# Kernel optimization log

Hardware: AMD Instinct MI355X
Metric: run time of the kernel (lower is better)

Reference implementation:

```python
import jax, jax.numpy as jnp
import numpy as np

B, HQ, HK, S, D, HID, BS = 2, 32, 8, 8192, 128, 128, 16
NB = S // BS  # 512 pooled blocks


def rotate_half(x):
    h = x.shape[-1] // 2
    return jnp.concatenate([-x[..., h:], x[..., :h]], axis=-1)


def pool_cat(x):
    # avg + max pooling over block_size along the sequence dim, concat on feature dim
    b, h, s, d = x.shape
    xb = x.reshape(b, h, s // BS, BS, d)
    return jnp.concatenate([xb.mean(axis=3), xb.max(axis=3)], axis=-1)  # [b,h,NB,2d]


def setup_inputs() -> dict:
    key = jax.random.key(0)
    k0, k1, k2, k3 = jax.random.split(key, 4)
    q = jax.random.normal(k0, (B, HQ, S, D), jnp.float32)
    k = jax.random.normal(k1, (B, HK, S, D), jnp.float32)
    wq = jax.random.normal(k2, (HQ, 2 * D, HID), jnp.float32) / np.float32(np.sqrt(2 * D))
    wk = jax.random.normal(k3, (HK, 2 * D, HID), jnp.float32) / np.float32(np.sqrt(2 * D))
    # causal block mask
    mask = jnp.broadcast_to(jnp.tril(jnp.ones((NB, NB), bool))[None, None], (B, 1, NB, NB))
    # RoPE tables over pooled positions
    pos = jnp.arange(NB, dtype=jnp.float32)
    inv_freq = 1.0 / (10000.0 ** (jnp.arange(0, HID, 2, dtype=jnp.float32) / HID))
    freqs = pos[:, None] * inv_freq[None, :]              # [NB, HID/2]
    emb = jnp.concatenate([freqs, freqs], axis=-1)        # [NB, HID]
    cos = jnp.broadcast_to(jnp.cos(emb)[None], (B, NB, HID))
    sin = jnp.broadcast_to(jnp.sin(emb)[None], (B, NB, HID))
    return {"q": q, "k": k, "attention_mask": mask, "cos": cos, "sin": sin, "wq": wq, "wk": wk}


def reference(q, k, attention_mask, cos, sin, wq, wk):
    # pooled multi-head linear projections
    qh = jnp.einsum('bhnc,hcd->bhnd', pool_cat(q), wq)   # [B,HQ,NB,HID]
    kh = jnp.einsum('bhnc,hcd->bhnd', pool_cat(k), wk)   # [B,HK,NB,HID]
    # RoPE (unsqueeze_dim=1)
    c, s = cos[:, None], sin[:, None]
    qh = qh * c + rotate_half(qh) * s
    kh = kh * c + rotate_half(kh) * s
    # GQA: repeat kv heads
    kh = jnp.repeat(kh, HQ // HK, axis=1)                # [B,HQ,NB,HID]
    attn = jnp.einsum('bhqd,bhkd->bhqk', qh, kh) / jnp.sqrt(jnp.float32(HID))
    attn = jnp.where(attention_mask, attn, jnp.float32(-1e9))
    return jax.nn.softmax(attn, axis=-1)
```

## Files before the change

### kernel.cpp

```cpp
#include <hip/hip_runtime.h>

namespace {
constexpr int BB  = 2;
constexpr int HQ  = 32;
constexpr int HK  = 8;
constexpr int S   = 8192;
constexpr int D   = 128;
constexpr int HID = 128;
constexpr int BS  = 16;
constexpr int NB  = 512;
constexpr int C2D = 256;
}

__global__ __launch_bounds__(256) void pool_gemm_rope_kernel(
    const float* __restrict__ qx, const float* __restrict__ kx,
    const float* __restrict__ wqp, const float* __restrict__ wkp,
    const float* __restrict__ cosp, const float* __restrict__ sinp,
    float* __restrict__ qh, float* __restrict__ kh)
{
  constexpr int PST = 260;
  constexpr int RST = 132;
  __shared__ float smem[32 * PST];

  const int t  = threadIdx.x;
  const int n0 = blockIdx.x * 32;
  const int hy = blockIdx.y;
  const int b  = blockIdx.z;

  const float* x; const float* w; float* o; int H; int h;
  if (hy < HQ) { x = qx; w = wqp; o = qh; H = HQ; h = hy; }
  else         { x = kx; w = wkp; o = kh; H = HK; h = hy - HQ; }

  const float* xb = x + (((size_t)b * H + h) * S + (size_t)n0 * BS) * D;
  for (int it = t; it < 32 * 32; it += 256) {
    const int m = it >> 5, d4 = it & 31;
    const float4* p = (const float4*)(xb + (size_t)m * BS * D) + d4;
    float4 v = p[0];
    float sx = v.x, sy = v.y, sz = v.z, sw = v.w;
    float mx = v.x, my = v.y, mz = v.z, mw = v.w;
#pragma unroll
    for (int i = 1; i < BS; ++i) {
      v = p[i * (D / 4)];
      sx += v.x; sy += v.y; sz += v.z; sw += v.w;
      mx = fmaxf(mx, v.x); my = fmaxf(my, v.y);
      mz = fmaxf(mz, v.z); mw = fmaxf(mw, v.w);
    }
    const float inv16 = 1.0f / 16.0f;
    *(float4*)&smem[m * PST + 4 * d4] =
        make_float4(sx * inv16, sy * inv16, sz * inv16, sw * inv16);
    *(float4*)&smem[m * PST + 128 + 4 * d4] = make_float4(mx, my, mz, mw);
  }
  __syncthreads();

  const int dt = t & 31, mt = t >> 5;
  const int d0 = dt * 4, m0 = mt * 4;
  const float* wb = w + (size_t)h * C2D * HID;
  float4 acc[4];
#pragma unroll
  for (int i = 0; i < 4; ++i) acc[i] = make_float4(0.f, 0.f, 0.f, 0.f);

  for (int c = 0; c < C2D; c += 4) {
    const float4 w0 = *(const float4*)(wb + (size_t)(c + 0) * HID + d0);
    const float4 w1 = *(const float4*)(wb + (size_t)(c + 1) * HID + d0);
    const float4 w2 = *(const float4*)(wb + (size_t)(c + 2) * HID + d0);
    const float4 w3 = *(const float4*)(wb + (size_t)(c + 3) * HID + d0);
#pragma unroll
    for (int i = 0; i < 4; ++i) {
      const float4 pv = *(const float4*)&smem[(m0 + i) * PST + c];
      acc[i].x += pv.x * w0.x + pv.y * w1.x + pv.z * w2.x + pv.w * w3.x;
      acc[i].y += pv.x * w0.y + pv.y * w1.y + pv.z * w2.y + pv.w * w3.y;
      acc[i].z += pv.x * w0.z + pv.y * w1.z + pv.z * w2.z + pv.w * w3.z;
      acc[i].w += pv.x * w0.w + pv.y * w1.w + pv.z * w2.w + pv.w * w3.w;
    }
  }
  __syncthreads();

#pragma unroll
  for (int i = 0; i < 4; ++i)
    *(float4*)&smem[(m0 + i) * RST + d0] = acc[i];
  __syncthreads();

  const float sgn = (d0 < 64) ? -1.0f : 1.0f;
#pragma unroll
  for (int i = 0; i < 4; ++i) {
    const int n = n0 + m0 + i;
    const float4 cv = *(const float4*)(cosp + ((size_t)b * NB + n) * HID + d0);
    const float4 sv = *(const float4*)(sinp + ((size_t)b * NB + n) * HID + d0);
    const float4 pr = *(const float4*)&smem[(m0 + i) * RST + (d0 ^ 64)];
    float4 ov;
    ov.x = acc[i].x * cv.x + sgn * pr.x * sv.x;
    ov.y = acc[i].y * cv.y + sgn * pr.y * sv.y;
    ov.z = acc[i].z * cv.z + sgn * pr.z * sv.z;
    ov.w = acc[i].w * cv.w + sgn * pr.w * sv.w;
    *(float4*)(o + (((size_t)b * H + h) * NB + n) * HID + d0) = ov;
  }
}

#define SWZ(r, d4) ((r) * 128 + ((((d4) ^ ((r) & 7))) << 2))

__global__ __launch_bounds__(256) void attn_exp_kernel(
    const float* __restrict__ qh, const float* __restrict__ kh,
    float* __restrict__ out, float* __restrict__ rinv)
{
  __shared__ float qs[64 * 128];
  __shared__ float ks[64 * 128];

  const int t = threadIdx.x;
  const int x = blockIdx.x;
  const int h = blockIdx.y;
  const int b = blockIdx.z;
  const int qg = t >> 4, kg = t & 15;
  const float scale = 0.08838834764831843f;

  const float* qbase = qh + (((size_t)b * HQ + h) * NB) * HID;
  const float* kbase = kh + (((size_t)b * HK + (h >> 2)) * NB) * HID;
  float* obase = out + (((size_t)b * HQ + h) * NB) * (size_t)NB;

  const int sq = qg & 7;
  const int sk = kg & 7;

  for (int sel = 0; sel < 2; ++sel) {
    const int qt = sel ? (7 - x) : x;
    __syncthreads();
    for (int it = t; it < 64 * 32; it += 256) {
      const int r = it >> 5, d4 = it & 31;
      *(float4*)&qs[SWZ(r, d4)] =
          *(const float4*)(qbase + ((size_t)(qt * 64 + r)) * HID + 4 * d4);
    }
    float rs[4] = {0.f, 0.f, 0.f, 0.f};

    for (int kt = 0; kt <= qt; ++kt) {
      __syncthreads();
      for (int it = t; it < 64 * 32; it += 256) {
        const int r = it >> 5, d4 = it & 31;
        *(float4*)&ks[SWZ(r, d4)] =
            *(const float4*)(kbase + ((size_t)(kt * 64 + r)) * HID + 4 * d4);
      }
      __syncthreads();

      float acc[4][4];
#pragma unroll
      for (int i = 0; i < 4; ++i)
#pragma unroll
        for (int j = 0; j < 4; ++j) acc[i][j] = 0.f;

      for (int d4 = 0; d4 < 32; ++d4) {
        const int xq = ((d4 ^ sq) << 2);
        const int xk = ((d4 ^ sk) << 2);
        float4 qv[4], kv[4];
#pragma unroll
        for (int i = 0; i < 4; ++i) qv[i] = *(const float4*)&qs[(qg + 16 * i) * 128 + xq];
#pragma unroll
        for (int j = 0; j < 4; ++j) kv[j] = *(const float4*)&ks[(kg + 16 * j) * 128 + xk];
#pragma unroll
        for (int i = 0; i < 4; ++i)
#pragma unroll
          for (int j = 0; j < 4; ++j)
            acc[i][j] += qv[i].x * kv[j].x + qv[i].y * kv[j].y +
                         qv[i].z * kv[j].z + qv[i].w * kv[j].w;
      }

      const bool diag = (kt == qt);
#pragma unroll
      for (int i = 0; i < 4; ++i) {
        const int qn = qt * 64 + qg + 16 * i;
#pragma unroll
        for (int j = 0; j < 4; ++j) {
          const int kn = kt * 64 + kg + 16 * j;
          float p = 0.0f;
          if (!diag || kn <= qn) p = __expf(acc[i][j] * scale);
          rs[i] += p;
          obase[(size_t)qn * NB + kn] = p;
        }
      }
    }

#pragma unroll
    for (int i = 0; i < 4; ++i) {
      float v = rs[i];
      v += __shfl_xor(v, 1, 64);
      v += __shfl_xor(v, 2, 64);
      v += __shfl_xor(v, 4, 64);
      v += __shfl_xor(v, 8, 64);
      if (kg == 0)
        rinv[((size_t)b * HQ + h) * NB + qt * 64 + qg + 16 * i] = 1.0f / v;
    }
  }
}

__global__ __launch_bounds__(128) void norm_kernel(
    float* __restrict__ out, const float* __restrict__ rinv)
{
  const int qn = blockIdx.x, h = blockIdx.y, b = blockIdx.z;
  const size_t row = ((size_t)b * HQ + h) * NB + qn;
  const float inv = rinv[row];
  const int klim4 = ((qn >> 6) + 1) * 16;
  float4* orow = (float4*)(out + row * NB);
  const int j = threadIdx.x;
  float4 v;
  if (j < klim4) {
    v = orow[j];
    v.x *= inv; v.y *= inv; v.z *= inv; v.w *= inv;
  } else {
    v = make_float4(0.f, 0.f, 0.f, 0.f);
  }
  orow[j] = v;
}

extern "C" void kernel_launch(void* const* d_in, const int* in_sizes, int n_in,
                              void* d_out, int out_size, void* d_ws, size_t ws_size,
                              hipStream_t stream)
{
  const float* q    = (const float*)d_in[0];
  const float* k    = (const float*)d_in[1];
  const float* cosp = (const float*)d_in[3];
  const float* sinp = (const float*)d_in[4];
  const float* wq   = (const float*)d_in[5];
  const float* wk   = (const float*)d_in[6];
  float* out = (float*)d_out;

  float* qh   = (float*)d_ws;
  float* kh   = qh + (size_t)BB * HQ * NB * HID;
  float* rinv = kh + (size_t)BB * HK * NB * HID;

  hipLaunchKernelGGL(pool_gemm_rope_kernel, dim3(NB / 32, HQ + HK, BB), dim3(256),
                     0, stream, q, k, wq, wk, cosp, sinp, qh, kh);
  hipLaunchKernelGGL(attn_exp_kernel, dim3(4, HQ, BB), dim3(256),
                     0, stream, qh, kh, out, rinv);
  hipLaunchKernelGGL(norm_kernel, dim3(NB, HQ, BB), dim3(128),
                     0, stream, out, rinv);
}
```

Baseline: 534.8 us.

## Use split-bf16 MFMA for attention scores and fuse normalization into attention kernel

The projection kernel now writes Q/K as hi+lo bf16 pairs, with the softmax scale folded into Q. The attention kernel computes scores with 16x16x32 bf16 MFMA using three products (hi*hi, hi*lo, lo*hi) to approximate fp32 accuracy. Row sums are reduced through LDS inside the block, and probabilities are kept in registers so they can be normalized before the single store. This removes the separate norm kernel and its re-read of the output. Work is split into 16-row strips paired for causal balance, and the masked region is zero-filled. The cost is a small precision loss from the split-bf16 approximation and scattered 4-byte output stores.

New measurement: 487.2 us. 8.9% less time.

```diff
diff --git a/kernel.cpp b/kernel.cpp
--- a/kernel.cpp
+++ b/kernel.cpp
@@ -10,13 +10,27 @@
 constexpr int BS  = 16;
 constexpr int NB  = 512;
 constexpr int C2D = 256;
+constexpr int RW  = 256;
+}
+
+typedef __attribute__((ext_vector_type(8))) short short8;
+typedef __attribute__((ext_vector_type(4))) float f32x4;
+
+__device__ inline unsigned short f2bf(float f) {
+  unsigned u = __builtin_bit_cast(unsigned, f);
+  unsigned r = u + 0x7fff + ((u >> 16) & 1);
+  return (unsigned short)(r >> 16);
+}
+__device__ inline float bf2f(unsigned short s) {
+  unsigned u = ((unsigned)s) << 16;
+  return __builtin_bit_cast(float, u);
 }
 
 __global__ __launch_bounds__(256) void pool_gemm_rope_kernel(
     const float* __restrict__ qx, const float* __restrict__ kx,
     const float* __restrict__ wqp, const float* __restrict__ wkp,
     const float* __restrict__ cosp, const float* __restrict__ sinp,
-    float* __restrict__ qh, float* __restrict__ kh)
+    unsigned short* __restrict__ qhb, unsigned short* __restrict__ khb)
 {
   constexpr int PST = 260;
   constexpr int RST = 132;
@@ -27,9 +41,9 @@
   const int hy = blockIdx.y;
   const int b  = blockIdx.z;
 
-  const float* x; const float* w; float* o; int H; int h;
-  if (hy < HQ) { x = qx; w = wqp; o = qh; H = HQ; h = hy; }
-  else         { x = kx; w = wkp; o = kh; H = HK; h = hy - HQ; }
+  const float* x; const float* w; unsigned short* o; int H; int h; bool isq;
+  if (hy < HQ) { x = qx; w = wqp; o = qhb; H = HQ; h = hy; isq = true; }
+  else         { x = kx; w = wkp; o = khb; H = HK; h = hy - HQ; isq = false; }
 
   const float* xb = x + (((size_t)b * H + h) * S + (size_t)n0 * BS) * D;
   for (int it = t; it < 32 * 32; it += 256) {
@@ -81,130 +95,135 @@
   __syncthreads();
 
   const float sgn = (d0 < 64) ? -1.0f : 1.0f;
+  const float qscale = isq ? 0.08838834764831843f : 1.0f;
 #pragma unroll
   for (int i = 0; i < 4; ++i) {
     const int n = n0 + m0 + i;
     const float4 cv = *(const float4*)(cosp + ((size_t)b * NB + n) * HID + d0);
     const float4 sv = *(const float4*)(sinp + ((size_t)b * NB + n) * HID + d0);
     const float4 pr = *(const float4*)&smem[(m0 + i) * RST + (d0 ^ 64)];
-    float4 ov;
-    ov.x = acc[i].x * cv.x + sgn * pr.x * sv.x;
-    ov.y = acc[i].y * cv.y + sgn * pr.y * sv.y;
-    ov.z = acc[i].z * cv.z + sgn * pr.z * sv.z;
-    ov.w = acc[i].w * cv.w + sgn * pr.w * sv.w;
-    *(float4*)(o + (((size_t)b * H + h) * NB + n) * HID + d0) = ov;
-  }
-}
-
-#define SWZ(r, d4) ((r) * 128 + ((((d4) ^ ((r) & 7))) << 2))
-
-__global__ __launch_bounds__(256) void attn_exp_kernel(
-    const float* __restrict__ qh, const float* __restrict__ kh,
-    float* __restrict__ out, float* __restrict__ rinv)
+    float ov[4];
+    ov[0] = (acc[i].x * cv.x + sgn * pr.x * sv.x) * qscale;
+    ov[1] = (acc[i].y * cv.y + sgn * pr.y * sv.y) * qscale;
+    ov[2] = (acc[i].z * cv.z + sgn * pr.z * sv.z) * qscale;
+    ov[3] = (acc[i].w * cv.w + sgn * pr.w * sv.w) * qscale;
+    ushort4 hi, lo;
+    hi.x = f2bf(ov[0]); lo.x = f2bf(ov[0] - bf2f(hi.x));
+    hi.y = f2bf(ov[1]); lo.y = f2bf(ov[1] - bf2f(hi.y));
+    hi.z = f2bf(ov[2]); lo.z = f2bf(ov[2] - bf2f(hi.z));
+    hi.w = f2bf(ov[3]); lo.w = f2bf(ov[3] - bf2f(hi.w));
+    unsigned short* orow = o + (((size_t)b * H + h) * NB + n) * RW + d0;
+    *(ushort4*)orow = hi;
+    *(ushort4*)(orow + 128) = lo;
+  }
+}
+
+__global__ __launch_bounds__(256) void attn_kernel(
+    const unsigned short* __restrict__ qhb,
+    const unsigned short* __restrict__ khb,
+    float* __restrict__ out)
 {
-  __shared__ float qs[64 * 128];
-  __shared__ float ks[64 * 128];
+  __shared__ float rs_lds[16];
 
   const int t = threadIdx.x;
+  const int w = t >> 6;
+  const int lane = t & 63;
+  const int col = lane & 15;
+  const int quad = lane >> 4;
   const int x = blockIdx.x;
   const int h = blockIdx.y;
   const int b = blockIdx.z;
-  const int qg = t >> 4, kg = t & 15;
-  const float scale = 0.08838834764831843f;
-
-  const float* qbase = qh + (((size_t)b * HQ + h) * NB) * HID;
-  const float* kbase = kh + (((size_t)b * HK + (h >> 2)) * NB) * HID;
+
+  const unsigned short* qbase = qhb + (((size_t)b * HQ + h) * NB) * RW;
+  const unsigned short* kbase = khb + (((size_t)b * HK + (h >> 2)) * NB) * RW;
   float* obase = out + (((size_t)b * HQ + h) * NB) * (size_t)NB;
 
-  const int sq = qg & 7;
-  const int sk = kg & 7;
-
-  for (int sel = 0; sel < 2; ++sel) {
-    const int qt = sel ? (7 - x) : x;
+  for (int ph = 0; ph < 2; ++ph) {
+    const int strip = ph ? (31 - x) : x;
+
     __syncthreads();
-    for (int it = t; it < 64 * 32; it += 256) {
-      const int r = it >> 5, d4 = it & 31;
-      *(float4*)&qs[SWZ(r, d4)] =
-          *(const float4*)(qbase + ((size_t)(qt * 64 + r)) * HID + 4 * d4);
-    }
+    if (t < 16) rs_lds[t] = 0.f;
+    __syncthreads();
+
+    const unsigned short* qrow = qbase + (size_t)(strip * 16 + col) * RW + quad * 8;
+    short8 qf[8];
+#pragma unroll
+    for (int f = 0; f < 4; ++f) {
+      qf[f]     = *(const short8*)(qrow + f * 32);
+      qf[4 + f] = *(const short8*)(qrow + f * 32 + 128);
+    }
+
+    const unsigned short* krow = kbase + (size_t)col * RW + quad * 8;
+    const int n = (w <= strip) ? ((strip - w) >> 2) + 1 : 0;
+
+    f32x4 pbuf[8];
     float rs[4] = {0.f, 0.f, 0.f, 0.f};
 
-    for (int kt = 0; kt <= qt; ++kt) {
-      __syncthreads();
-      for (int it = t; it < 64 * 32; it += 256) {
-        const int r = it >> 5, d4 = it & 31;
-        *(float4*)&ks[SWZ(r, d4)] =
-            *(const float4*)(kbase + ((size_t)(kt * 64 + r)) * HID + 4 * d4);
+#pragma unroll
+    for (int ti = 0; ti < 8; ++ti) {
+      if (ti < n) {
+        const int k16 = w + 4 * ti;
+        const unsigned short* kr = krow + (size_t)k16 * 16 * RW;
+        short8 kf[8];
+#pragma unroll
+        for (int f = 0; f < 4; ++f) {
+          kf[f]     = *(const short8*)(kr + f * 32);
+          kf[4 + f] = *(const short8*)(kr + f * 32 + 128);
+        }
+        f32x4 acc = {0.f, 0.f, 0.f, 0.f};
+#pragma unroll
+        for (int f = 0; f < 4; ++f) {
+          acc = __builtin_amdgcn_mfma_f32_16x16x32_bf16(qf[f],     kf[f],     acc, 0, 0, 0);
+          acc = __builtin_amdgcn_mfma_f32_16x16x32_bf16(qf[f],     kf[4 + f], acc, 0, 0, 0);
+          acc = __builtin_amdgcn_mfma_f32_16x16x32_bf16(qf[4 + f], kf[f],     acc, 0, 0, 0);
+        }
+        const bool diag = (k16 == strip);
+        f32x4 p;
+#pragma unroll
+        for (int r = 0; r < 4; ++r) {
+          float v = __expf(acc[r]);
+          if (diag && col > quad * 4 + r) v = 0.f;
+          p[r] = v;
+          rs[r] += v;
+        }
+        pbuf[ti] = p;
       }
-      __syncthreads();
-
-      float acc[4][4];
-#pragma unroll
-      for (int i = 0; i < 4; ++i)
-#pragma unroll
-        for (int j = 0; j < 4; ++j) acc[i][j] = 0.f;
-
-      for (int d4 = 0; d4 < 32; ++d4) {
-        const int xq = ((d4 ^ sq) << 2);
-        const int xk = ((d4 ^ sk) << 2);
-        float4 qv[4], kv[4];
-#pragma unroll
-        for (int i = 0; i < 4; ++i) qv[i] = *(const float4*)&qs[(qg + 16 * i) * 128 + xq];
-#pragma unroll
-        for (int j = 0; j < 4; ++j) kv[j] = *(const float4*)&ks[(kg + 16 * j) * 128 + xk];
-#pragma unroll
-        for (int i = 0; i < 4; ++i)
-#pragma unroll
-          for (int j = 0; j < 4; ++j)
-            acc[i][j] += qv[i].x * kv[j].x + qv[i].y * kv[j].y +
-                         qv[i].z * kv[j].z + qv[i].w * kv[j].w;
-      }
-
-      const bool diag = (kt == qt);
-#pragma unroll
-      for (int i = 0; i < 4; ++i) {
-        const int qn = qt * 64 + qg + 16 * i;
-#pragma unroll
-        for (int j = 0; j < 4; ++j) {
-          const int kn = kt * 64 + kg + 16 * j;
-          float p = 0.0f;
-          if (!diag || kn <= qn) p = __expf(acc[i][j] * scale);
-          rs[i] += p;
-          obase[(size_t)qn * NB + kn] = p;
-        }
-      }
-    }
-
-#pragma unroll
-    for (int i = 0; i < 4; ++i) {
-      float v = rs[i];
+    }
+
+#pragma unroll
+    for (int r = 0; r < 4; ++r) {
+      float v = rs[r];
       v += __shfl_xor(v, 1, 64);
       v += __shfl_xor(v, 2, 64);
       v += __shfl_xor(v, 4, 64);
       v += __shfl_xor(v, 8, 64);
-      if (kg == 0)
-        rinv[((size_t)b * HQ + h) * NB + qt * 64 + qg + 16 * i] = 1.0f / v;
-    }
-  }
-}
-
-__global__ __launch_bounds__(128) void norm_kernel(
-    float* __restrict__ out, const float* __restrict__ rinv)
-{
-  const int qn = blockIdx.x, h = blockIdx.y, b = blockIdx.z;
-  const size_t row = ((size_t)b * HQ + h) * NB + qn;
-  const float inv = rinv[row];
-  const int klim4 = ((qn >> 6) + 1) * 16;
-  float4* orow = (float4*)(out + row * NB);
-  const int j = threadIdx.x;
-  float4 v;
-  if (j < klim4) {
-    v = orow[j];
-    v.x *= inv; v.y *= inv; v.z *= inv; v.w *= inv;
-  } else {
-    v = make_float4(0.f, 0.f, 0.f, 0.f);
-  }
-  orow[j] = v;
+      if (col == 0) atomicAdd(&rs_lds[quad * 4 + r], v);
+    }
+
+    {
+      const int r = t & 15;
+      const float4 z = make_float4(0.f, 0.f, 0.f, 0.f);
+      for (int c4 = (strip + 1) * 4 + (t >> 4); c4 < 128; c4 += 16)
+        *(float4*)(obase + (size_t)(strip * 16 + r) * NB + 4 * c4) = z;
+    }
+
+    __syncthreads();
+
+    float inv[4];
+#pragma unroll
+    for (int r = 0; r < 4; ++r) inv[r] = 1.0f / rs_lds[quad * 4 + r];
+
+#pragma unroll
+    for (int ti = 0; ti < 8; ++ti) {
+      if (ti < n) {
+        const int k16 = w + 4 * ti;
+#pragma unroll
+        for (int r = 0; r < 4; ++r)
+          obase[(size_t)(strip * 16 + quad * 4 + r) * NB + k16 * 16 + col] =
+              pbuf[ti][r] * inv[r];
+      }
+    }
+  }
 }
 
 extern "C" void kernel_launch(void* const* d_in, const int* in_sizes, int n_in,
@@ -219,14 +238,11 @@
   const float* wk   = (const float*)d_in[6];
   float* out = (float*)d_out;
 
-  float* qh   = (float*)d_ws;
-  float* kh   = qh + (size_t)BB * HQ * NB * HID;
-  float* rinv = kh + (size_t)BB * HK * NB * HID;
+  unsigned short* qhb = (unsigned short*)d_ws;
+  unsigned short* khb = qhb + (size_t)BB * HQ * NB * RW;
 
   hipLaunchKernelGGL(pool_gemm_rope_kernel, dim3(NB / 32, HQ + HK, BB), dim3(256),
-                     0, stream, q, k, wq, wk, cosp, sinp, qh, kh);
-  hipLaunchKernelGGL(attn_exp_kernel, dim3(4, HQ, BB), dim3(256),
-                     0, stream, qh, kh, out, rinv);
-  hipLaunchKernelGGL(norm_kernel, dim3(NB, HQ, BB), dim3(128),
-                     0, stream, out, rinv);
-}
+                     0, stream, q, k, wq, wk, cosp, sinp, qhb, khb);
+  hipLaunchKernelGGL(attn_kernel, dim3(16, HQ, BB), dim3(256),
+                     0, stream, qhb, khb, out);
+}
```
